# Kernel optimization log

Measured on AMD Instinct MI355X. Metric: run time of the kernel, lower is better.

## Reference

```python
import jax, jax.numpy as jnp
import numpy as np

B = 1048576

def _mlp3(x, W1, b1, W2, b2, W3, b3):
    # x: [..., d] -> [..., 1]; Linear(d,d)+ReLU, Linear(d,d)+ReLU, Linear(d,1)
    h = jax.nn.relu(jnp.einsum('...d,od->...o', x, W1) + b1)
    h = jax.nn.relu(jnp.einsum('...d,od->...o', h, W2) + b2)
    return jnp.einsum('...d,od->...o', h, W3) + b3

def setup_inputs() -> dict:
    key = jax.random.key(0)
    ks = jax.random.split(key, 20)
    def lin(k, out_d, in_d):
        bound = 1.0 / np.sqrt(in_d)
        k1, k2 = jax.random.split(k)
        W = jax.random.uniform(k1, (out_d, in_d), jnp.float32, -bound, bound)
        b = jax.random.uniform(k2, (out_d,), jnp.float32, -bound, bound)
        return W, b
    inp = {
        'edge': jax.random.normal(ks[0], (B, 4, 10), jnp.float32),
        'cross': jax.random.normal(ks[1], (B, 4, 8), jnp.float32),
        'corner': jax.random.normal(ks[2], (B, 4, 10), jnp.float32),
        'cn': jax.random.normal(ks[3], (B, 1), jnp.float32),
    }
    eW1, eb1 = lin(ks[4], 10, 10); eW2, eb2 = lin(ks[5], 10, 10); eW3, eb3 = lin(ks[6], 1, 10)
    xW1, xb1 = lin(ks[7], 8, 8);  xW2, xb2 = lin(ks[8], 8, 8);  xW3, xb3 = lin(ks[9], 1, 8)
    cW1, cb1 = lin(ks[10], 10, 10); cW2, cb2 = lin(ks[11], 10, 10); cW3, cb3 = lin(ks[12], 1, 10)
    nW, nb = lin(ks[13], 1, 1)
    inp.update(dict(eW1=eW1, eb1=eb1, eW2=eW2, eb2=eb2, eW3=eW3, eb3=eb3,
                    xW1=xW1, xb1=xb1, xW2=xW2, xb2=xb2, xW3=xW3, xb3=xb3,
                    cW1=cW1, cb1=cb1, cW2=cW2, cb2=cb2, cW3=cW3, cb3=cb3,
                    nW=nW, nb=nb))
    return inp

def reference(edge, cross, corner, cn,
              eW1, eb1, eW2, eb2, eW3, eb3,
              xW1, xb1, xW2, xb2, xW3, xb3,
              cW1, cb1, cW2, cb2, cW3, cb3,
              nW, nb) -> jnp.ndarray:
    # Shared-weight MLP over each of the 4 slices, summed over the slice dim.
    e = _mlp3(edge, eW1, eb1, eW2, eb2, eW3, eb3).sum(axis=1)    # [B,1]
    x = _mlp3(cross, xW1, xb1, xW2, xb2, xW3, xb3).sum(axis=1)   # [B,1]
    c = _mlp3(corner, cW1, cb1, cW2, cb2, cW3, cb3).sum(axis=1)  # [B,1]
    n = jnp.einsum('bd,od->bo', cn, nW) + nb                     # [B,1]
    return e + x + c + n
```

## Files before the change

kernel.cpp:

```cpp
#include <hip/hip_runtime.h>


#define OFF_EW1 0
#define OFF_EW2 120
#define OFF_CW1 240
#define OFF_CW2 360
#define OFF_XW1 480
#define OFF_XW2 544
#define OFF_EW3 608
#define OFF_CW3 618
#define OFF_XW3 628
#define OFF_EB1 636
#define OFF_EB2 646
#define OFF_CB1 656
#define OFF_CB2 666
#define OFF_XB1 676
#define OFF_XB2 684
#define OFF_SC  692
#define SMEM_TOT 700

template<int D, int P>
__device__ __forceinline__ float mlp3_sum4(const float* __restrict__ x,
                                           const float* __restrict__ W1,
                                           const float* __restrict__ b1,
                                           const float* __restrict__ W2,
                                           const float* __restrict__ b2,
                                           const float* __restrict__ W3,
                                           float b3)
{
    float h1[4 * D];
    #pragma unroll
    for (int o = 0; o < D; ++o) {
        float w[D];
        #pragma unroll
        for (int i = 0; i < D; ++i) w[i] = W1[o * P + i];
        const float bb = b1[o];
        #pragma unroll
        for (int s = 0; s < 4; ++s) {
            float acc = bb;
            #pragma unroll
            for (int i = 0; i < D; ++i) acc = fmaf(w[i], x[s * D + i], acc);
            h1[s * D + o] = fmaxf(acc, 0.0f);
        }
    }
    float h2[4 * D];
    #pragma unroll
    for (int o = 0; o < D; ++o) {
        float w[D];
        #pragma unroll
        for (int i = 0; i < D; ++i) w[i] = W2[o * P + i];
        const float bb = b2[o];
        #pragma unroll
        for (int s = 0; s < 4; ++s) {
            float acc = bb;
            #pragma unroll
            for (int i = 0; i < D; ++i) acc = fmaf(w[i], h1[s * D + i], acc);
            h2[s * D + o] = fmaxf(acc, 0.0f);
        }
    }
    float out = 4.0f * b3;
    #pragma unroll
    for (int i = 0; i < D; ++i) {
        const float w = W3[i];
        #pragma unroll
        for (int s = 0; s < 4; ++s) out = fmaf(w, h2[s * D + i], out);
    }
    return out;
}

__global__ __launch_bounds__(256)
void osero_kernel(const float* __restrict__ edge,
                  const float* __restrict__ cross_,
                  const float* __restrict__ corner,
                  const float* __restrict__ cn,
                  const float* __restrict__ eW1, const float* __restrict__ eb1,
                  const float* __restrict__ eW2, const float* __restrict__ eb2,
                  const float* __restrict__ eW3, const float* __restrict__ eb3,
                  const float* __restrict__ xW1, const float* __restrict__ xb1,
                  const float* __restrict__ xW2, const float* __restrict__ xb2,
                  const float* __restrict__ xW3, const float* __restrict__ xb3,
                  const float* __restrict__ cW1, const float* __restrict__ cb1,
                  const float* __restrict__ cW2, const float* __restrict__ cb2,
                  const float* __restrict__ cW3, const float* __restrict__ cb3,
                  const float* __restrict__ nW,  const float* __restrict__ nb,
                  float* __restrict__ out, int nelem)
{
    __shared__ __align__(16) float sm[SMEM_TOT];
    const int t = threadIdx.x;

    for (int idx = t; idx < 120; idx += 256) {
        int r = idx / 12, c = idx - r * 12;
        sm[OFF_EW1 + idx] = (c < 10) ? eW1[r * 10 + c] : 0.0f;
    }
    for (int idx = t; idx < 120; idx += 256) {
        int r = idx / 12, c = idx - r * 12;
        sm[OFF_EW2 + idx] = (c < 10) ? eW2[r * 10 + c] : 0.0f;
    }
    for (int idx = t; idx < 120; idx += 256) {
        int r = idx / 12, c = idx - r * 12;
        sm[OFF_CW1 + idx] = (c < 10) ? cW1[r * 10 + c] : 0.0f;
    }
    for (int idx = t; idx < 120; idx += 256) {
        int r = idx / 12, c = idx - r * 12;
        sm[OFF_CW2 + idx] = (c < 10) ? cW2[r * 10 + c] : 0.0f;
    }
    if (t < 64)  sm[OFF_XW1 + t] = xW1[t];
    if (t >= 64 && t < 128) sm[OFF_XW2 + (t - 64)] = xW2[t - 64];
    if (t < 10) {
        sm[OFF_EW3 + t] = eW3[t];
        sm[OFF_CW3 + t] = cW3[t];
        sm[OFF_EB1 + t] = eb1[t];
        sm[OFF_EB2 + t] = eb2[t];
        sm[OFF_CB1 + t] = cb1[t];
        sm[OFF_CB2 + t] = cb2[t];
    }
    if (t < 8) {
        sm[OFF_XW3 + t] = xW3[t];
        sm[OFF_XB1 + t] = xb1[t];
        sm[OFF_XB2 + t] = xb2[t];
    }
    if (t == 0) {
        sm[OFF_SC + 0] = eb3[0];
        sm[OFF_SC + 1] = cb3[0];
        sm[OFF_SC + 2] = xb3[0];
        sm[OFF_SC + 3] = nW[0];
        sm[OFF_SC + 4] = nb[0];
    }
    __syncthreads();

    const int b = blockIdx.x * 256 + t;
    if (b >= nelem) return;

    float xe[40];
    {
        const float4* p = reinterpret_cast<const float4*>(edge) + (size_t)b * 10;
        #pragma unroll
        for (int j = 0; j < 10; ++j) {
            float4 v = p[j];
            xe[4 * j + 0] = v.x; xe[4 * j + 1] = v.y;
            xe[4 * j + 2] = v.z; xe[4 * j + 3] = v.w;
        }
    }
    float xx[32];
    {
        const float4* p = reinterpret_cast<const float4*>(cross_) + (size_t)b * 8;
        #pragma unroll
        for (int j = 0; j < 8; ++j) {
            float4 v = p[j];
            xx[4 * j + 0] = v.x; xx[4 * j + 1] = v.y;
            xx[4 * j + 2] = v.z; xx[4 * j + 3] = v.w;
        }
    }
    float xc[40];
    {
        const float4* p = reinterpret_cast<const float4*>(corner) + (size_t)b * 10;
        #pragma unroll
        for (int j = 0; j < 10; ++j) {
            float4 v = p[j];
            xc[4 * j + 0] = v.x; xc[4 * j + 1] = v.y;
            xc[4 * j + 2] = v.z; xc[4 * j + 3] = v.w;
        }
    }
    const float cnv = cn[b];

    const float e  = mlp3_sum4<10, 12>(xe, sm + OFF_EW1, sm + OFF_EB1,
                                           sm + OFF_EW2, sm + OFF_EB2,
                                           sm + OFF_EW3, sm[OFF_SC + 0]);
    const float xr = mlp3_sum4<8, 8>  (xx, sm + OFF_XW1, sm + OFF_XB1,
                                           sm + OFF_XW2, sm + OFF_XB2,
                                           sm + OFF_XW3, sm[OFF_SC + 2]);
    const float cr = mlp3_sum4<10, 12>(xc, sm + OFF_CW1, sm + OFF_CB1,
                                           sm + OFF_CW2, sm + OFF_CB2,
                                           sm + OFF_CW3, sm[OFF_SC + 1]);
    const float n  = fmaf(cnv, sm[OFF_SC + 3], sm[OFF_SC + 4]);

    out[b] = e + xr + cr + n;
}

extern "C" void kernel_launch(void* const* d_in, const int* in_sizes, int n_in,
                              void* d_out, int out_size, void* d_ws, size_t ws_size,
                              hipStream_t stream) {
    const float* edge   = (const float*)d_in[0];
    const float* cross_ = (const float*)d_in[1];
    const float* corner = (const float*)d_in[2];
    const float* cn     = (const float*)d_in[3];
    const float* eW1 = (const float*)d_in[4];
    const float* eb1 = (const float*)d_in[5];
    const float* eW2 = (const float*)d_in[6];
    const float* eb2 = (const float*)d_in[7];
    const float* eW3 = (const float*)d_in[8];
    const float* eb3 = (const float*)d_in[9];
    const float* xW1 = (const float*)d_in[10];
    const float* xb1 = (const float*)d_in[11];
    const float* xW2 = (const float*)d_in[12];
    const float* xb2 = (const float*)d_in[13];
    const float* xW3 = (const float*)d_in[14];
    const float* xb3 = (const float*)d_in[15];
    const float* cW1 = (const float*)d_in[16];
    const float* cb1 = (const float*)d_in[17];
    const float* cW2 = (const float*)d_in[18];
    const float* cb2 = (const float*)d_in[19];
    const float* cW3 = (const float*)d_in[20];
    const float* cb3 = (const float*)d_in[21];
    const float* nW  = (const float*)d_in[22];
    const float* nb  = (const float*)d_in[23];

    const int nelem = in_sizes[3];
    const int grid  = (nelem + 255) / 256;

    osero_kernel<<<grid, 256, 0, stream>>>(edge, cross_, corner, cn,
                                           eW1, eb1, eW2, eb2, eW3, eb3,
                                           xW1, xb1, xW2, xb2, xW3, xb3,
                                           cW1, cb1, cW2, cb2, cW3, cb3,
                                           nW, nb,
                                           (float*)d_out, nelem);
}
```

Before: 463.0 us.

## Split branches across grid.y, stage inputs through LDS, use packed FMA with atomics

Splits the three MLP branches across a 3-wide grid.y so each block handles one branch. Each block stages its input tile into LDS with coalesced float4 loads instead of per-thread strided loads. The math uses packed 2-wide FMA over output pairs, with weights read directly from global memory as uniform loads. Partial results are combined through atomic adds onto an output zeroed by a memset, which adds a memset launch, atomic traffic and non-deterministic summation order, and drops the bounds check.

```diff
diff --git a/kernel.cpp b/kernel.cpp
--- a/kernel.cpp
+++ b/kernel.cpp
@@ -1,71 +1,74 @@
 #include <hip/hip_runtime.h>
 
 
-#define OFF_EW1 0
-#define OFF_EW2 120
-#define OFF_CW1 240
-#define OFF_CW2 360
-#define OFF_XW1 480
-#define OFF_XW2 544
-#define OFF_EW3 608
-#define OFF_CW3 618
-#define OFF_XW3 628
-#define OFF_EB1 636
-#define OFF_EB2 646
-#define OFF_CB1 656
-#define OFF_CB2 666
-#define OFF_XB1 676
-#define OFF_XB2 684
-#define OFF_SC  692
-#define SMEM_TOT 700
+typedef float f2 __attribute__((ext_vector_type(2)));
 
-template<int D, int P>
-__device__ __forceinline__ float mlp3_sum4(const float* __restrict__ x,
-                                           const float* __restrict__ W1,
-                                           const float* __restrict__ b1,
-                                           const float* __restrict__ W2,
-                                           const float* __restrict__ b2,
-                                           const float* __restrict__ W3,
-                                           float b3)
+template<int F4, int PSTR>
+__device__ __forceinline__ void stage(const float* __restrict__ in,
+                                      float* __restrict__ sm, int t, int blk)
 {
-    float h1[4 * D];
+    const float4* src = reinterpret_cast<const float4*>(in) + (size_t)blk * (256 * F4);
     #pragma unroll
-    for (int o = 0; o < D; ++o) {
-        float w[D];
+    for (int it = 0; it < F4; ++it) {
+        const int g = it * 256 + t;
+        float4 v = src[g];
+        const int e = g / F4;
+        const int j = g - e * F4;
+        *reinterpret_cast<float4*>(sm + e * PSTR + j * 4) = v;
+    }
+}
+
+template<int D>
+__device__ __forceinline__ float mlp4(const float* __restrict__ xl,
+                                      const float* __restrict__ W1,
+                                      const float* __restrict__ b1,
+                                      const float* __restrict__ W2,
+                                      const float* __restrict__ b2,
+                                      const float* __restrict__ W3,
+                                      const float* __restrict__ b3)
+{
+    constexpr int H = D / 2;
+    f2 oacc = {0.0f, 0.0f};
+    #pragma unroll
+    for (int s = 0; s < 4; ++s) {
+        f2 xs[H];
         #pragma unroll
-        for (int i = 0; i < D; ++i) w[i] = W1[o * P + i];
-        const float bb = b1[o];
+        for (int k = 0; k < H; ++k)
+            xs[k] = *reinterpret_cast<const f2*>(xl + s * D + 2 * k);
+
+        f2 h1[H];
         #pragma unroll
-        for (int s = 0; s < 4; ++s) {
-            float acc = bb;
+        for (int op = 0; op < H; ++op) {
+            f2 a = {b1[2 * op], b1[2 * op + 1]};
             #pragma unroll
-            for (int i = 0; i < D; ++i) acc = fmaf(w[i], x[s * D + i], acc);
-            h1[s * D + o] = fmaxf(acc, 0.0f);
+            for (int i = 0; i < D; ++i) {
+                const float xv = (i & 1) ? xs[i >> 1].y : xs[i >> 1].x;
+                const f2 w = {W1[(2 * op) * D + i], W1[(2 * op + 1) * D + i]};
+                a = __builtin_elementwise_fma(w, (f2){xv, xv}, a);
+            }
+            h1[op] = __builtin_elementwise_max(a, (f2){0.0f, 0.0f});
+        }
+
+        f2 h2[H];
+        #pragma unroll
+        for (int op = 0; op < H; ++op) {
+            f2 a = {b2[2 * op], b2[2 * op + 1]};
+            #pragma unroll
+            for (int i = 0; i < D; ++i) {
+                const float hv = (i & 1) ? h1[i >> 1].y : h1[i >> 1].x;
+                const f2 w = {W2[(2 * op) * D + i], W2[(2 * op + 1) * D + i]};
+                a = __builtin_elementwise_fma(w, (f2){hv, hv}, a);
+            }
+            h2[op] = __builtin_elementwise_max(a, (f2){0.0f, 0.0f});
+        }
+
+        #pragma unroll
+        for (int k = 0; k < H; ++k) {
+            const f2 w3 = {W3[2 * k], W3[2 * k + 1]};
+            oacc = __builtin_elementwise_fma(w3, h2[k], oacc);
         }
     }
-    float h2[4 * D];
-    #pragma unroll
-    for (int o = 0; o < D; ++o) {
-        float w[D];
-        #pragma unroll
-        for (int i = 0; i < D; ++i) w[i] = W2[o * P + i];
-        const float bb = b2[o];
-        #pragma unroll
-        for (int s = 0; s < 4; ++s) {
-            float acc = bb;
-            #pragma unroll
-            for (int i = 0; i < D; ++i) acc = fmaf(w[i], h1[s * D + i], acc);
-            h2[s * D + o] = fmaxf(acc, 0.0f);
-        }
-    }
-    float out = 4.0f * b3;
-    #pragma unroll
-    for (int i = 0; i < D; ++i) {
-        const float w = W3[i];
-        #pragma unroll
-        for (int s = 0; s < 4; ++s) out = fmaf(w, h2[s * D + i], out);
-    }
-    return out;
+    return oacc.x + oacc.y + 4.0f * b3[0];
 }
 
 __global__ __launch_bounds__(256)
@@ -83,98 +86,32 @@
                   const float* __restrict__ cW2, const float* __restrict__ cb2,
                   const float* __restrict__ cW3, const float* __restrict__ cb3,
                   const float* __restrict__ nW,  const float* __restrict__ nb,
-                  float* __restrict__ out, int nelem)
+                  float* __restrict__ out)
 {
-    __shared__ __align__(16) float sm[SMEM_TOT];
-    const int t = threadIdx.x;
+    __shared__ __align__(16) float sm[256 * 44];
 
-    for (int idx = t; idx < 120; idx += 256) {
-        int r = idx / 12, c = idx - r * 12;
-        sm[OFF_EW1 + idx] = (c < 10) ? eW1[r * 10 + c] : 0.0f;
+    const int t   = threadIdx.x;
+    const int blk = blockIdx.x;
+    const int y   = blockIdx.y;
+    const int b   = blk * 256 + t;
+
+    float val;
+    if (y == 0) {
+        stage<10, 44>(edge, sm, t, blk);
+        __syncthreads();
+        val = mlp4<10>(sm + t * 44, eW1, eb1, eW2, eb2, eW3, eb3);
+    } else if (y == 1) {
+        stage<10, 44>(corner, sm, t, blk);
+        __syncthreads();
+        val = mlp4<10>(sm + t * 44, cW1, cb1, cW2, cb2, cW3, cb3);
+    } else {
+        stage<8, 36>(cross_, sm, t, blk);
+        __syncthreads();
+        val = mlp4<8>(sm + t * 36, xW1, xb1, xW2, xb2, xW3, xb3);
+        val += fmaf(cn[b], nW[0], nb[0]);
     }
-    for (int idx = t; idx < 120; idx += 256) {
-        int r = idx / 12, c = idx - r * 12;
-        sm[OFF_EW2 + idx] = (c < 10) ? eW2[r * 10 + c] : 0.0f;
-    }
-    for (int idx = t; idx < 120; idx += 256) {
-        int r = idx / 12, c = idx - r * 12;
-        sm[OFF_CW1 + idx] = (c < 10) ? cW1[r * 10 + c] : 0.0f;
-    }
-    for (int idx = t; idx < 120; idx += 256) {
-        int r = idx / 12, c = idx - r * 12;
-        sm[OFF_CW2 + idx] = (c < 10) ? cW2[r * 10 + c] : 0.0f;
-    }
-    if (t < 64)  sm[OFF_XW1 + t] = xW1[t];
-    if (t >= 64 && t < 128) sm[OFF_XW2 + (t - 64)] = xW2[t - 64];
-    if (t < 10) {
-        sm[OFF_EW3 + t] = eW3[t];
-        sm[OFF_CW3 + t] = cW3[t];
-        sm[OFF_EB1 + t] = eb1[t];
-        sm[OFF_EB2 + t] = eb2[t];
-        sm[OFF_CB1 + t] = cb1[t];
-        sm[OFF_CB2 + t] = cb2[t];
-    }
-    if (t < 8) {
-        sm[OFF_XW3 + t] = xW3[t];
-        sm[OFF_XB1 + t] = xb1[t];
-        sm[OFF_XB2 + t] = xb2[t];
-    }
-    if (t == 0) {
-        sm[OFF_SC + 0] = eb3[0];
-        sm[OFF_SC + 1] = cb3[0];
-        sm[OFF_SC + 2] = xb3[0];
-        sm[OFF_SC + 3] = nW[0];
-        sm[OFF_SC + 4] = nb[0];
-    }
-    __syncthreads();
 
-    const int b = blockIdx.x * 256 + t;
-    if (b >= nelem) return;
-
-    float xe[40];
-    {
-        const float4* p = reinterpret_cast<const float4*>(edge) + (size_t)b * 10;
-        #pragma unroll
-        for (int j = 0; j < 10; ++j) {
-            float4 v = p[j];
-            xe[4 * j + 0] = v.x; xe[4 * j + 1] = v.y;
-            xe[4 * j + 2] = v.z; xe[4 * j + 3] = v.w;
-        }
-    }
-    float xx[32];
-    {
-        const float4* p = reinterpret_cast<const float4*>(cross_) + (size_t)b * 8;
-        #pragma unroll
-        for (int j = 0; j < 8; ++j) {
-            float4 v = p[j];
-            xx[4 * j + 0] = v.x; xx[4 * j + 1] = v.y;
-            xx[4 * j + 2] = v.z; xx[4 * j + 3] = v.w;
-        }
-    }
-    float xc[40];
-    {
-        const float4* p = reinterpret_cast<const float4*>(corner) + (size_t)b * 10;
-        #pragma unroll
-        for (int j = 0; j < 10; ++j) {
-            float4 v = p[j];
-            xc[4 * j + 0] = v.x; xc[4 * j + 1] = v.y;
-            xc[4 * j + 2] = v.z; xc[4 * j + 3] = v.w;
-        }
-    }
-    const float cnv = cn[b];
-
-    const float e  = mlp3_sum4<10, 12>(xe, sm + OFF_EW1, sm + OFF_EB1,
-                                           sm + OFF_EW2, sm + OFF_EB2,
-                                           sm + OFF_EW3, sm[OFF_SC + 0]);
-    const float xr = mlp3_sum4<8, 8>  (xx, sm + OFF_XW1, sm + OFF_XB1,
-                                           sm + OFF_XW2, sm + OFF_XB2,
-                                           sm + OFF_XW3, sm[OFF_SC + 2]);
-    const float cr = mlp3_sum4<10, 12>(xc, sm + OFF_CW1, sm + OFF_CB1,
-                                           sm + OFF_CW2, sm + OFF_CB2,
-                                           sm + OFF_CW3, sm[OFF_SC + 1]);
-    const float n  = fmaf(cnv, sm[OFF_SC + 3], sm[OFF_SC + 4]);
-
-    out[b] = e + xr + cr + n;
+    unsafeAtomicAdd(out + b, val);
 }
 
 extern "C" void kernel_launch(void* const* d_in, const int* in_sizes, int n_in,
@@ -206,12 +143,14 @@
     const float* nb  = (const float*)d_in[23];
 
     const int nelem = in_sizes[3];
-    const int grid  = (nelem + 255) / 256;
+    const int nblk  = (nelem + 255) / 256;
 
+    hipMemsetAsync(d_out, 0, (size_t)out_size * sizeof(float), stream);
+
+    dim3 grid(nblk, 3);
     osero_kernel<<<grid, 256, 0, stream>>>(edge, cross_, corner, cn,
                                            eW1, eb1, eW2, eb2, eW3, eb3,
                                            xW1, xb1, xW2, xb2, xW3, xb3,
                                            cW1, cb1, cW2, cb2, cW3, cb3,
-                                           nW, nb,
-                                           (float*)d_out, nelem);
+                                           nW, nb, (float*)d_out);
 }
```

Result: faster. 452.2 us (-2.3%).
